# Kernel optimization log

Measured on AMD Instinct MI355X. Metric: run time of the kernel, lower is better.

## Reference

```python
import jax, jax.numpy as jnp
import numpy as np

N_NODES = 100000
N_EDGES = 1600000


def _leaky_relu(x, slope=0.1):
    return jnp.where(x > 0, x, slope * x)


def _sage_conv(x, src, dst, Wl, Wr, b, n_nodes):
    # mean aggregation of source messages onto target nodes (PyG SAGEConv, aggr='mean')
    msg = x[src]                                              # [E, d] gather
    agg_sum = jax.ops.segment_sum(msg, dst, num_segments=n_nodes)
    cnt = jax.ops.segment_sum(jnp.ones((src.shape[0],), x.dtype), dst, num_segments=n_nodes)
    agg = agg_sum / jnp.maximum(cnt, 1.0)[:, None]            # empty neighborhoods -> 0
    # out = lin_l(agg) + lin_r(x); bias lives in lin_l
    return agg @ Wl + x @ Wr + b


def setup_inputs() -> dict:
    key = jax.random.key(0)
    ks = jax.random.split(key, 8)
    x = jax.random.normal(ks[0], (N_NODES, 128), dtype=jnp.float32)
    edge_index = jax.random.randint(ks[1], (2, N_EDGES), 0, N_NODES, dtype=jnp.int32)
    scale = 0.05
    Wl_stack = jax.random.normal(ks[2], (3, 128, 128), dtype=jnp.float32) * scale
    Wr_stack = jax.random.normal(ks[3], (3, 128, 128), dtype=jnp.float32) * scale
    b_stack = jax.random.normal(ks[4], (3, 128), dtype=jnp.float32) * scale
    Wl_out = jax.random.normal(ks[5], (128, 64), dtype=jnp.float32) * scale
    Wr_out = jax.random.normal(ks[6], (128, 64), dtype=jnp.float32) * scale
    b_out = jax.random.normal(ks[7], (64,), dtype=jnp.float32) * scale
    return {"x": x, "edge_index": edge_index, "Wl_stack": Wl_stack,
            "Wr_stack": Wr_stack, "b_stack": b_stack,
            "Wl_out": Wl_out, "Wr_out": Wr_out, "b_out": b_out}


def reference(x, edge_index, Wl_stack, Wr_stack, b_stack, Wl_out, Wr_out, b_out):
    src, dst = edge_index[0], edge_index[1]
    n = x.shape[0]
    h = x
    # conv1 + hidden convs, each followed by LeakyReLU(0.1)
    for i in range(Wl_stack.shape[0]):
        h = _leaky_relu(_sage_conv(h, src, dst, Wl_stack[i], Wr_stack[i], b_stack[i], n))
    # final SAGEConv without activation
    out = _sage_conv(h, src, dst, Wl_out, Wr_out, b_out, n)
    return out
```

## Files before the change

kernel.cpp:

```cpp
#include <hip/hip_runtime.h>

#define NN 100000
#define NNP 100096
#define NE 1600000
#define NBK 391
#define CAP 4608
#define SCCH 4096
#define NSC ((NE + SCCH - 1) / SCCH)

typedef __attribute__((ext_vector_type(8))) short bf16x8;
typedef __attribute__((ext_vector_type(4))) float f32x4;

__device__ __forceinline__ float bf2f(unsigned short u) {
    unsigned int v = ((unsigned int)u) << 16;
    return __builtin_bit_cast(float, v);
}
__device__ __forceinline__ unsigned short f2bf(float f) {
    unsigned int u = __builtin_bit_cast(unsigned int, f);
    u += 0x7FFFu + ((u >> 16) & 1u);
    return (unsigned short)(u >> 16);
}
__device__ __forceinline__ unsigned int pk2(float lo, float hi) {
    return (unsigned int)f2bf(lo) | ((unsigned int)f2bf(hi) << 16);
}
__device__ __forceinline__ float bflo(unsigned int v) {
    return __builtin_bit_cast(float, v << 16);
}
__device__ __forceinline__ float bfhi(unsigned int v) {
    return __builtin_bit_cast(float, v & 0xFFFF0000u);
}


__global__ __launch_bounds__(256) void kb_init(int* __restrict__ bcur) {
    int i = blockIdx.x * 256 + threadIdx.x;
    if (i < NBK) bcur[i] = i * CAP;
}

__global__ __launch_bounds__(256) void kb_scatter(const int* __restrict__ src,
                                                  const int* __restrict__ dst,
                                                  int* __restrict__ bcur,
                                                  unsigned int* __restrict__ ebuf) {
    __shared__ int lh[NBK], lbase[NBK];
    int tid = threadIdx.x;
    for (int i = tid; i < NBK; i += 256) lh[i] = 0;
    __syncthreads();
    int base = blockIdx.x * SCCH;
    int lim = min(SCCH, NE - base);
    for (int i = tid; i < lim; i += 256)
        atomicAdd(&lh[dst[base + i] >> 8], 1);
    __syncthreads();
    for (int i = tid; i < NBK; i += 256)
        lbase[i] = lh[i] ? atomicAdd(&bcur[i], lh[i]) : 0;
    __syncthreads();
    for (int i = tid; i < NBK; i += 256) lh[i] = 0;
    __syncthreads();
    for (int i = tid; i < lim; i += 256) {
        int d = dst[base + i];
        int s = src[base + i];
        int b = d >> 8;
        int off = atomicAdd(&lh[b], 1);
        ebuf[(size_t)lbase[b] + off] = ((unsigned)s << 8) | (unsigned)(d & 255);
    }
}

__global__ __launch_bounds__(256) void kb_csr(const unsigned int* __restrict__ ebuf,
                                              const int* __restrict__ bcur,
                                              int* __restrict__ row_beg,
                                              int* __restrict__ row_end,
                                              int* __restrict__ csr) {
    __shared__ int sdeg[256], spre[256];
    int bkt = blockIdx.x;
    int tid = threadIdx.x;
    int nbase = bkt << 8;
    int ebeg = bkt * CAP;
    int eend = bcur[bkt];
    sdeg[tid] = 0;
    __syncthreads();
    for (int e = ebeg + tid; e < eend; e += 256)
        atomicAdd(&sdeg[ebuf[e] & 255], 1);
    __syncthreads();
    spre[tid] = sdeg[tid];
    __syncthreads();
#pragma unroll
    for (int off = 1; off < 256; off <<= 1) {
        int t = (tid >= off) ? spre[tid - off] : 0;
        __syncthreads();
        if (tid >= off) spre[tid] += t;
        __syncthreads();
    }
    int excl = spre[tid] - sdeg[tid];
    if (nbase + tid < NN) {
        row_beg[nbase + tid] = ebeg + excl;
        row_end[nbase + tid] = ebeg + excl + sdeg[tid];
    }
    __syncthreads();
    sdeg[tid] = excl;
    __syncthreads();
    for (int e = ebeg + tid; e < eend; e += 256) {
        unsigned int v = ebuf[e];
        int p = atomicAdd(&sdeg[v & 255], 1);
        csr[ebeg + p] = (int)(v >> 8);
    }
}


__global__ __launch_bounds__(256) void k_prep_wt(const float* __restrict__ Wl_stack,
                                                 const float* __restrict__ Wr_stack,
                                                 const float* __restrict__ Wl_out,
                                                 const float* __restrict__ Wr_out,
                                                 unsigned short* __restrict__ WT) {
    int i = blockIdx.x * 256 + threadIdx.x;
    const int L3OFF = 3 * 256 * 128;
    const int TOT = L3OFF + 128 * 128;
    if (i >= TOT) return;
    float v;
    if (i < L3OFF) {
        int l = i / (256 * 128);
        int r = i % (256 * 128);
        int c = r / 128;
        int k = r % 128;
        v = (c < 128) ? Wl_stack[(size_t)(l * 128 + k) * 128 + c]
                      : Wr_stack[(size_t)(l * 128 + k) * 128 + (c - 128)];
    } else {
        int r = i - L3OFF;
        int c = r / 128;
        int k = r % 128;
        v = (c < 64) ? Wl_out[(size_t)k * 64 + c]
                     : Wr_out[(size_t)k * 64 + (c - 64)];
    }
    WT[i] = f2bf(v);
}


template <int NOUT, bool F32IN>
__global__ __launch_bounds__(256) void k_mm(const void* __restrict__ Ain,
                                            const unsigned short* __restrict__ WT,
                                            unsigned short* __restrict__ Y,
                                            unsigned short* __restrict__ Z) {
    constexpr int HALVES = NOUT / 64;
    __shared__ unsigned char lds[32768];

    int tid = threadIdx.x;
    int wave = tid >> 6, l = tid & 63;
    int lrow = l & 15, g = l >> 4;
    int half = (HALVES == 2) ? (blockIdx.x & 1) : 0;
    int rowblk = (HALVES == 2) ? (blockIdx.x >> 1) : blockIdx.x;
    int rbase = rowblk * 256 + wave * 64;

    {
        const unsigned char* wsrc = (const unsigned char*)(WT + (size_t)half * 128 * 128);
#pragma unroll
        for (int j = 0; j < 8; ++j) {
            int lin = (j * 256 + tid) * 16;
            uint4 v = *(const uint4*)(wsrc + lin);
            int row = lin >> 8;
            int colb = lin & 255;
            *(uint4*)(lds + row * 256 + (colb ^ ((row & 7) << 4))) = v;
        }
    }

    bf16x8 af[4][4];
#pragma unroll
    for (int s = 0; s < 4; ++s) {
        int row = rbase + s * 16 + lrow;
#pragma unroll
        for (int ks = 0; ks < 4; ++ks) {
            if (F32IN) {
                int rc = row < NN ? row : NN - 1;
                const float* ap = (const float*)Ain + (size_t)rc * 128 + ks * 32 + g * 8;
                float4 a = *(const float4*)ap;
                float4 b = *(const float4*)(ap + 4);
                uint4 u;
                u.x = pk2(a.x, a.y); u.y = pk2(a.z, a.w);
                u.z = pk2(b.x, b.y); u.w = pk2(b.z, b.w);
                af[s][ks] = __builtin_bit_cast(bf16x8, u);
            } else {
                af[s][ks] = *(const bf16x8*)((const unsigned short*)Ain
                                             + (size_t)row * 128 + ks * 32 + g * 8);
            }
        }
    }
    __syncthreads();

#pragma unroll
    for (int cg = 0; cg < 8; ++cg) {
        int c0 = cg * 16;
        int rl = c0 + lrow;
        bf16x8 bfr[4];
#pragma unroll
        for (int ks = 0; ks < 4; ++ks) {
            int colb = ks * 64 + g * 16;
            bfr[ks] = *(const bf16x8*)(lds + rl * 256 + (colb ^ ((rl & 7) << 4)));
        }
        int gc0 = half * 128 + c0;
        unsigned short* dstp = (gc0 < NOUT) ? Y : Z;
        int cb = ((gc0 < NOUT) ? gc0 : gc0 - NOUT) + g * 4;
#pragma unroll
        for (int s = 0; s < 4; ++s) {
            f32x4 acc = {0.f, 0.f, 0.f, 0.f};
#pragma unroll
            for (int ks = 0; ks < 4; ++ks)
                acc = __builtin_amdgcn_mfma_f32_16x16x32_bf16(bfr[ks], af[s][ks], acc, 0, 0, 0);
            int row = rbase + s * 16 + lrow;
            uint2 w;
            w.x = pk2(acc[0], acc[1]);
            w.y = pk2(acc[2], acc[3]);
            *(uint2*)(dstp + (size_t)row * NOUT + cb) = w;
        }
    }
}


template <int NOUT, bool RELU>
__global__ __launch_bounds__(256) void k_aggb(const unsigned short* __restrict__ Y,
                                              const unsigned short* __restrict__ Z,
                                              const int* __restrict__ row_beg,
                                              const int* __restrict__ row_end,
                                              const int* __restrict__ csr,
                                              const float* __restrict__ b,
                                              unsigned short* __restrict__ outb,
                                              float* __restrict__ outf) {
    int lane = threadIdx.x & 63;
    int n = __builtin_amdgcn_readfirstlane(blockIdx.x * 4 + (threadIdx.x >> 6));
    if (n >= NN) return;
    int beg = __builtin_amdgcn_readfirstlane(row_beg[n]);
    int end = __builtin_amdgcn_readfirstlane(row_end[n]);
    float inv = (end > beg) ? 1.0f / (float)(end - beg) : 0.0f;

    if (NOUT == 128) {
        const int lane2 = lane * 2;
        float a0 = 0.f, a1 = 0.f;
        int e = beg;
        for (; e + 8 <= end; e += 8) {
            int s0 = csr[e + 0], s1 = csr[e + 1], s2 = csr[e + 2], s3 = csr[e + 3];
            int s4 = csr[e + 4], s5 = csr[e + 5], s6 = csr[e + 6], s7 = csr[e + 7];
            unsigned int v0 = *(const unsigned int*)(Y + (size_t)s0 * 128 + lane2);
            unsigned int v1 = *(const unsigned int*)(Y + (size_t)s1 * 128 + lane2);
            unsigned int v2 = *(const unsigned int*)(Y + (size_t)s2 * 128 + lane2);
            unsigned int v3 = *(const unsigned int*)(Y + (size_t)s3 * 128 + lane2);
            unsigned int v4 = *(const unsigned int*)(Y + (size_t)s4 * 128 + lane2);
            unsigned int v5 = *(const unsigned int*)(Y + (size_t)s5 * 128 + lane2);
            unsigned int v6 = *(const unsigned int*)(Y + (size_t)s6 * 128 + lane2);
            unsigned int v7 = *(const unsigned int*)(Y + (size_t)s7 * 128 + lane2);
            a0 += bflo(v0) + bflo(v1) + bflo(v2) + bflo(v3)
                + bflo(v4) + bflo(v5) + bflo(v6) + bflo(v7);
            a1 += bfhi(v0) + bfhi(v1) + bfhi(v2) + bfhi(v3)
                + bfhi(v4) + bfhi(v5) + bfhi(v6) + bfhi(v7);
        }
        for (; e + 4 <= end; e += 4) {
            int s0 = csr[e + 0], s1 = csr[e + 1], s2 = csr[e + 2], s3 = csr[e + 3];
            unsigned int v0 = *(const unsigned int*)(Y + (size_t)s0 * 128 + lane2);
            unsigned int v1 = *(const unsigned int*)(Y + (size_t)s1 * 128 + lane2);
            unsigned int v2 = *(const unsigned int*)(Y + (size_t)s2 * 128 + lane2);
            unsigned int v3 = *(const unsigned int*)(Y + (size_t)s3 * 128 + lane2);
            a0 += bflo(v0) + bflo(v1) + bflo(v2) + bflo(v3);
            a1 += bfhi(v0) + bfhi(v1) + bfhi(v2) + bfhi(v3);
        }
        for (; e < end; ++e) {
            int s = csr[e];
            unsigned int v = *(const unsigned int*)(Y + (size_t)s * 128 + lane2);
            a0 += bflo(v);
            a1 += bfhi(v);
        }
        unsigned int zv = *(const unsigned int*)(Z + (size_t)n * 128 + lane2);
        float2 bb = *(const float2*)(b + lane2);
        float o0 = a0 * inv + bflo(zv) + bb.x;
        float o1 = a1 * inv + bfhi(zv) + bb.y;
        if (RELU) {
            o0 = o0 > 0.f ? o0 : 0.1f * o0;
            o1 = o1 > 0.f ? o1 : 0.1f * o1;
        }
        *(unsigned int*)(outb + (size_t)n * 128 + lane2) = pk2(o0, o1);
    } else {
        float a0 = 0.f;
        int e = beg;
        for (; e + 8 <= end; e += 8) {
            int s0 = csr[e + 0], s1 = csr[e + 1], s2 = csr[e + 2], s3 = csr[e + 3];
            int s4 = csr[e + 4], s5 = csr[e + 5], s6 = csr[e + 6], s7 = csr[e + 7];
            float f0 = bf2f(Y[(size_t)s0 * 64 + lane]);
            float f1 = bf2f(Y[(size_t)s1 * 64 + lane]);
            float f2 = bf2f(Y[(size_t)s2 * 64 + lane]);
            float f3 = bf2f(Y[(size_t)s3 * 64 + lane]);
            float f4 = bf2f(Y[(size_t)s4 * 64 + lane]);
            float f5 = bf2f(Y[(size_t)s5 * 64 + lane]);
            float f6 = bf2f(Y[(size_t)s6 * 64 + lane]);
            float f7 = bf2f(Y[(size_t)s7 * 64 + lane]);
            a0 += f0 + f1 + f2 + f3 + f4 + f5 + f6 + f7;
        }
        for (; e + 4 <= end; e += 4) {
            int s0 = csr[e + 0], s1 = csr[e + 1], s2 = csr[e + 2], s3 = csr[e + 3];
            float f0 = bf2f(Y[(size_t)s0 * 64 + lane]);
            float f1 = bf2f(Y[(size_t)s1 * 64 + lane]);
            float f2 = bf2f(Y[(size_t)s2 * 64 + lane]);
            float f3 = bf2f(Y[(size_t)s3 * 64 + lane]);
            a0 += f0 + f1 + f2 + f3;
        }
        for (; e < end; ++e) {
            int s = csr[e];
            a0 += bf2f(Y[(size_t)s * 64 + lane]);
        }
        float o = a0 * inv + bf2f(Z[(size_t)n * 64 + lane]) + b[lane];
        if (RELU) o = o > 0.f ? o : 0.1f * o;
        outf[(size_t)n * 64 + lane] = o;
    }
}


extern "C" void kernel_launch(void* const* d_in, const int* in_sizes, int n_in,
                              void* d_out, int out_size, void* d_ws, size_t ws_size,
                              hipStream_t stream) {
    const float* x        = (const float*)d_in[0];
    const int*   ei       = (const int*)d_in[1];
    const float* Wl_stack = (const float*)d_in[2];
    const float* Wr_stack = (const float*)d_in[3];
    const float* b_stack  = (const float*)d_in[4];
    const float* Wl_out   = (const float*)d_in[5];
    const float* Wr_out   = (const float*)d_in[6];
    const float* b_out    = (const float*)d_in[7];
    float* out = (float*)d_out;

    unsigned short* hb = (unsigned short*)d_ws;
    unsigned short* Yb = hb + (size_t)NNP * 128;
    unsigned short* Zb = Yb + (size_t)NNP * 128;
    unsigned short* WT = Zb + (size_t)NNP * 128;
    unsigned int* ebuf = (unsigned int*)(WT + 114688);
    int* csr     = (int*)(ebuf + (size_t)NBK * CAP);
    int* row_beg = csr + (size_t)NBK * CAP;
    int* row_end = row_beg + NN;
    int* bcur    = row_end + NN;

    const int* src = ei;
    const int* dst = ei + NE;

    kb_init<<<(NBK + 255) / 256, 256, 0, stream>>>(bcur);
    kb_scatter<<<NSC, 256, 0, stream>>>(src, dst, bcur, ebuf);
    kb_csr<<<NBK, 256, 0, stream>>>(ebuf, bcur, row_beg, row_end, csr);

    k_prep_wt<<<448, 256, 0, stream>>>(Wl_stack, Wr_stack, Wl_out, Wr_out, WT);

    k_mm<128, true><<<(NNP / 256) * 2, 256, 0, stream>>>(x, WT, Yb, Zb);
    k_aggb<128, true><<<(NN + 3) / 4, 256, 0, stream>>>(Yb, Zb, row_beg, row_end, csr,
                                                        b_stack, hb, nullptr);
    for (int l = 1; l < 3; ++l) {
        k_mm<128, false><<<(NNP / 256) * 2, 256, 0, stream>>>(hb, WT + l * 32768, Yb, Zb);
        k_aggb<128, true><<<(NN + 3) / 4, 256, 0, stream>>>(Yb, Zb, row_beg, row_end, csr,
                                                            b_stack + l * 128, hb, nullptr);
    }
    k_mm<64, false><<<NNP / 256, 256, 0, stream>>>(hb, WT + 98304, Yb, Zb);
    k_aggb<64, false><<<(NN + 3) / 4, 256, 0, stream>>>(Yb, Zb, row_beg, row_end, csr,
                                                        b_out, nullptr, out);
}
```

Baseline: 381.1 us.

## Fuse edge scatter with first-layer matmul and merge prep kernels, remap MM blocks per XCD

```diff
diff --git a/kernel.cpp b/kernel.cpp
--- a/kernel.cpp
+++ b/kernel.cpp
@@ -7,6 +7,7 @@
 #define CAP 4608
 #define SCCH 4096
 #define NSC ((NE + SCCH - 1) / SCCH)
+#define MMG 782
 
 typedef __attribute__((ext_vector_type(8))) short bf16x8;
 typedef __attribute__((ext_vector_type(4))) float f32x4;
@@ -30,21 +31,60 @@
     return __builtin_bit_cast(float, v & 0xFFFF0000u);
 }
 
-
-__global__ __launch_bounds__(256) void kb_init(int* __restrict__ bcur) {
+__device__ __forceinline__ int mm_gmap(int bid, int off) {
+    int x = (bid + off) & 7;
+    int j = bid >> 3;
+    int g = j;
+#pragma unroll
+    for (int u = 0; u < 8; ++u)
+        if (u < x) g += ((((u - off) & 7) < 6) ? 98 : 97);
+    return g;
+}
+
+
+__global__ __launch_bounds__(256) void k_prep(const float* __restrict__ Wl_stack,
+                                              const float* __restrict__ Wr_stack,
+                                              const float* __restrict__ Wl_out,
+                                              const float* __restrict__ Wr_out,
+                                              unsigned short* __restrict__ WT,
+                                              int* __restrict__ bcur) {
     int i = blockIdx.x * 256 + threadIdx.x;
-    if (i < NBK) bcur[i] = i * CAP;
-}
-
-__global__ __launch_bounds__(256) void kb_scatter(const int* __restrict__ src,
-                                                  const int* __restrict__ dst,
-                                                  int* __restrict__ bcur,
-                                                  unsigned int* __restrict__ ebuf) {
-    __shared__ int lh[NBK], lbase[NBK];
-    int tid = threadIdx.x;
+    const int L3OFF = 3 * 256 * 128;
+    const int TOT = L3OFF + 128 * 128;
+    if (i < TOT) {
+        float v;
+        if (i < L3OFF) {
+            int l = i / (256 * 128);
+            int r = i % (256 * 128);
+            int c = r / 128;
+            int k = r % 128;
+            v = (c < 128) ? Wl_stack[(size_t)(l * 128 + k) * 128 + c]
+                          : Wr_stack[(size_t)(l * 128 + k) * 128 + (c - 128)];
+        } else {
+            int r = i - L3OFF;
+            int c = r / 128;
+            int k = r % 128;
+            v = (c < 64) ? Wl_out[(size_t)k * 64 + c]
+                         : Wr_out[(size_t)k * 64 + (c - 64)];
+        }
+        WT[i] = f2bf(v);
+    } else if (i - TOT < NBK) {
+        bcur[i - TOT] = (i - TOT) * CAP;
+    }
+}
+
+
+__device__ __forceinline__ void scatter_body(int bid, int tid,
+                                             const int* __restrict__ src,
+                                             const int* __restrict__ dst,
+                                             int* __restrict__ bcur,
+                                             unsigned int* __restrict__ ebuf,
+                                             unsigned char* smem) {
+    int* lh = (int*)smem;
+    int* lbase = lh + NBK;
     for (int i = tid; i < NBK; i += 256) lh[i] = 0;
     __syncthreads();
-    int base = blockIdx.x * SCCH;
+    int base = bid * SCCH;
     int lim = min(SCCH, NE - base);
     for (int i = tid; i < lim; i += 256)
         atomicAdd(&lh[dst[base + i] >> 8], 1);
@@ -63,88 +103,25 @@
     }
 }
 
-__global__ __launch_bounds__(256) void kb_csr(const unsigned int* __restrict__ ebuf,
-                                              const int* __restrict__ bcur,
-                                              int* __restrict__ row_beg,
-                                              int* __restrict__ row_end,
-                                              int* __restrict__ csr) {
-    __shared__ int sdeg[256], spre[256];
-    int bkt = blockIdx.x;
-    int tid = threadIdx.x;
-    int nbase = bkt << 8;
-    int ebeg = bkt * CAP;
-    int eend = bcur[bkt];
-    sdeg[tid] = 0;
-    __syncthreads();
-    for (int e = ebeg + tid; e < eend; e += 256)
-        atomicAdd(&sdeg[ebuf[e] & 255], 1);
-    __syncthreads();
-    spre[tid] = sdeg[tid];
-    __syncthreads();
-#pragma unroll
-    for (int off = 1; off < 256; off <<= 1) {
-        int t = (tid >= off) ? spre[tid - off] : 0;
-        __syncthreads();
-        if (tid >= off) spre[tid] += t;
-        __syncthreads();
-    }
-    int excl = spre[tid] - sdeg[tid];
-    if (nbase + tid < NN) {
-        row_beg[nbase + tid] = ebeg + excl;
-        row_end[nbase + tid] = ebeg + excl + sdeg[tid];
-    }
-    __syncthreads();
-    sdeg[tid] = excl;
-    __syncthreads();
-    for (int e = ebeg + tid; e < eend; e += 256) {
-        unsigned int v = ebuf[e];
-        int p = atomicAdd(&sdeg[v & 255], 1);
-        csr[ebeg + p] = (int)(v >> 8);
-    }
-}
-
-
-__global__ __launch_bounds__(256) void k_prep_wt(const float* __restrict__ Wl_stack,
-                                                 const float* __restrict__ Wr_stack,
-                                                 const float* __restrict__ Wl_out,
-                                                 const float* __restrict__ Wr_out,
-                                                 unsigned short* __restrict__ WT) {
-    int i = blockIdx.x * 256 + threadIdx.x;
-    const int L3OFF = 3 * 256 * 128;
-    const int TOT = L3OFF + 128 * 128;
-    if (i >= TOT) return;
-    float v;
-    if (i < L3OFF) {
-        int l = i / (256 * 128);
-        int r = i % (256 * 128);
-        int c = r / 128;
-        int k = r % 128;
-        v = (c < 128) ? Wl_stack[(size_t)(l * 128 + k) * 128 + c]
-                      : Wr_stack[(size_t)(l * 128 + k) * 128 + (c - 128)];
-    } else {
-        int r = i - L3OFF;
-        int c = r / 128;
-        int k = r % 128;
-        v = (c < 64) ? Wl_out[(size_t)k * 64 + c]
-                     : Wr_out[(size_t)k * 64 + (c - 64)];
-    }
-    WT[i] = f2bf(v);
-}
-
-
 template <int NOUT, bool F32IN>
-__global__ __launch_bounds__(256) void k_mm(const void* __restrict__ Ain,
-                                            const unsigned short* __restrict__ WT,
-                                            unsigned short* __restrict__ Y,
-                                            unsigned short* __restrict__ Z) {
+__device__ __forceinline__ void mm_body(int bid, int xoff, int tid,
+                                        const void* __restrict__ Ain,
+                                        const unsigned short* __restrict__ WT,
+                                        unsigned short* __restrict__ Y,
+                                        unsigned short* __restrict__ Z,
+                                        unsigned char* lds) {
     constexpr int HALVES = NOUT / 64;
-    __shared__ unsigned char lds[32768];
-
-    int tid = threadIdx.x;
     int wave = tid >> 6, l = tid & 63;
     int lrow = l & 15, g = l >> 4;
-    int half = (HALVES == 2) ? (blockIdx.x & 1) : 0;
-    int rowblk = (HALVES == 2) ? (blockIdx.x >> 1) : blockIdx.x;
+    int half, rowblk;
+    if (HALVES == 2) {
+        int gm = mm_gmap(bid, xoff);
+        half = gm & 1;
+        rowblk = gm >> 1;
+    } else {
+        half = 0;
+        rowblk = bid;
+    }
     int rbase = rowblk * 256 + wave * 64;
 
     {
@@ -207,6 +184,75 @@
             w.y = pk2(acc[2], acc[3]);
             *(uint2*)(dstp + (size_t)row * NOUT + cb) = w;
         }
+    }
+}
+
+
+__global__ __launch_bounds__(256) void k_fused0(const int* __restrict__ src,
+                                                const int* __restrict__ dst,
+                                                int* __restrict__ bcur,
+                                                unsigned int* __restrict__ ebuf,
+                                                const float* __restrict__ x,
+                                                const unsigned short* __restrict__ WT,
+                                                unsigned short* __restrict__ Y,
+                                                unsigned short* __restrict__ Z) {
+    __shared__ unsigned char smem[32768];
+    int tid = threadIdx.x;
+    if (blockIdx.x < NSC) {
+        scatter_body(blockIdx.x, tid, src, dst, bcur, ebuf, smem);
+    } else {
+        mm_body<128, true>(blockIdx.x - NSC, 7, tid, x, WT, Y, Z, smem);
+    }
+}
+
+
+template <int NOUT>
+__global__ __launch_bounds__(256) void k_mm(const unsigned short* __restrict__ Ain,
+                                            const unsigned short* __restrict__ WT,
+                                            unsigned short* __restrict__ Y,
+                                            unsigned short* __restrict__ Z) {
+    __shared__ unsigned char lds[32768];
+    mm_body<NOUT, false>(blockIdx.x, 0, threadIdx.x, Ain, WT, Y, Z, lds);
+}
+
+
+__global__ __launch_bounds__(256) void kb_csr(const unsigned int* __restrict__ ebuf,
+                                              const int* __restrict__ bcur,
+                                              int* __restrict__ row_beg,
+                                              int* __restrict__ row_end,
+                                              int* __restrict__ csr) {
+    __shared__ int sdeg[256], spre[256];
+    int bkt = blockIdx.x;
+    int tid = threadIdx.x;
+    int nbase = bkt << 8;
+    int ebeg = bkt * CAP;
+    int eend = bcur[bkt];
+    sdeg[tid] = 0;
+    __syncthreads();
+    for (int e = ebeg + tid; e < eend; e += 256)
+        atomicAdd(&sdeg[ebuf[e] & 255], 1);
+    __syncthreads();
+    spre[tid] = sdeg[tid];
+    __syncthreads();
+#pragma unroll
+    for (int off = 1; off < 256; off <<= 1) {
+        int t = (tid >= off) ? spre[tid - off] : 0;
+        __syncthreads();
+        if (tid >= off) spre[tid] += t;
+        __syncthreads();
+    }
+    int excl = spre[tid] - sdeg[tid];
+    if (nbase + tid < NN) {
+        row_beg[nbase + tid] = ebeg + excl;
+        row_end[nbase + tid] = ebeg + excl + sdeg[tid];
+    }
+    __syncthreads();
+    sdeg[tid] = excl;
+    __syncthreads();
+    for (int e = ebeg + tid; e < eend; e += 256) {
+        unsigned int v = ebuf[e];
+        int p = atomicAdd(&sdeg[v & 255], 1);
+        csr[ebeg + p] = (int)(v >> 8);
     }
 }
 
@@ -332,21 +378,19 @@
     const int* src = ei;
     const int* dst = ei + NE;
 
-    kb_init<<<(NBK + 255) / 256, 256, 0, stream>>>(bcur);
-    kb_scatter<<<NSC, 256, 0, stream>>>(src, dst, bcur, ebuf);
+    k_prep<<<450, 256, 0, stream>>>(Wl_stack, Wr_stack, Wl_out, Wr_out, WT, bcur);
+
+    k_fused0<<<NSC + MMG, 256, 0, stream>>>(src, dst, bcur, ebuf, x, WT, Yb, Zb);
+
     kb_csr<<<NBK, 256, 0, stream>>>(ebuf, bcur, row_beg, row_end, csr);
-
-    k_prep_wt<<<448, 256, 0, stream>>>(Wl_stack, Wr_stack, Wl_out, Wr_out, WT);
-
-    k_mm<128, true><<<(NNP / 256) * 2, 256, 0, stream>>>(x, WT, Yb, Zb);
     k_aggb<128, true><<<(NN + 3) / 4, 256, 0, stream>>>(Yb, Zb, row_beg, row_end, csr,
                                                         b_stack, hb, nullptr);
     for (int l = 1; l < 3; ++l) {
-        k_mm<128, false><<<(NNP / 256) * 2, 256, 0, stream>>>(hb, WT + l * 32768, Yb, Zb);
+        k_mm<128><<<MMG, 256, 0, stream>>>(hb, WT + l * 32768, Yb, Zb);
         k_aggb<128, true><<<(NN + 3) / 4, 256, 0, stream>>>(Yb, Zb, row_beg, row_end, csr,
                                                             b_stack + l * 128, hb, nullptr);
     }
-    k_mm<64, false><<<NNP / 256, 256, 0, stream>>>(hb, WT + 98304, Yb, Zb);
+    k_mm<64><<<NNP / 256, 256, 0, stream>>>(hb, WT + 98304, Yb, Zb);
     k_aggb<64, false><<<(NN + 3) / 4, 256, 0, stream>>>(Yb, Zb, row_beg, row_end, csr,
                                                         b_out, nullptr, out);
 }
```

Result: faster. 358.2 us (-6.0%).
